# Kernel optimization log

Measured on AMD Instinct MI355X. Metric: run time of the kernel, lower is better.

Reference implementation:

```python
import jax, jax.numpy as jnp
import numpy as np

B, T, E = 2, 2048, 1024
H = 16
D = E // H  # head_dim = 64


def setup_inputs() -> dict:
    key = jax.random.key(0)
    k1, k2, k3 = jax.random.split(key, 3)
    x = jax.random.normal(k1, (B, T, E), dtype=jnp.float32)
    w_qkv = jax.random.normal(k2, (3 * E, E), dtype=jnp.float32) * 0.02
    w_proj = jax.random.normal(k3, (E, E), dtype=jnp.float32) * 0.02
    return {"x": x, "w_qkv": w_qkv, "w_proj": w_proj}


def reference(x, w_qkv, w_proj):
    b, t, c = x.shape
    # qkv projection (torch Linear: x @ W^T), split into q,k,v
    qkv = jnp.einsum('btc,fc->btf', x, w_qkv)  # [B,T,3E]
    q, k, v = jnp.split(qkv, 3, axis=-1)
    # [B,T,E] -> [B,H,T,D]
    q = q.reshape(b, t, H, D).transpose(0, 2, 1, 3)
    k = k.reshape(b, t, H, D).transpose(0, 2, 1, 3)
    v = v.reshape(b, t, H, D).transpose(0, 2, 1, 3)
    scale = 1.0 / jnp.sqrt(jnp.float32(D))
    att = jnp.einsum('bhqd,bhkd->bhqk', q, k) * scale  # [B,H,T,T]
    causal = jnp.tril(jnp.ones((t, t), dtype=bool))
    att = jnp.where(causal[None, None], att, -jnp.inf)
    att = jax.nn.softmax(att, axis=-1)
    out = jnp.einsum('bhqk,bhkd->bhqd', att, v)  # [B,H,T,D]
    out = out.transpose(0, 2, 1, 3).reshape(b, t, c)  # [B,T,E]
    out = jnp.einsum('btc,oc->bto', out, w_proj)
    return out
```

## Files before the change

kernel.cpp:

```cpp
#include <hip/hip_runtime.h>
#include <stdint.h>
#include <stddef.h>

typedef __attribute__((ext_vector_type(8))) short s16x8;
typedef __attribute__((ext_vector_type(4))) short s16x4;
typedef __attribute__((ext_vector_type(4))) float f32x4;

#define B_  2
#define T_  2048
#define E_  1024
#define H_  16
#define E3_ 3072

__device__ __forceinline__ short f2bf(float f) {
  union { float f; uint32_t u; } v; v.f = f;
  uint32_t u = v.u;
  return (short)((u + 0x7FFFu + ((u >> 16) & 1u)) >> 16);
}

__device__ __forceinline__ void gload_lds16(const short* g, short* l) {
  __builtin_amdgcn_global_load_lds(
      (__attribute__((address_space(1))) void*)(const_cast<short*>(g)),
      (__attribute__((address_space(3))) void*)(l), 16, 0, 0);
}

__global__ void castk(const float* __restrict__ in, short* __restrict__ out, int n4) {
  const int i = blockIdx.x * 256 + threadIdx.x;
  if (i >= n4) return;
  const float4 v = ((const float4*)in)[i];
  s16x4 o;
  o[0] = f2bf(v.x); o[1] = f2bf(v.y); o[2] = f2bf(v.z); o[3] = f2bf(v.w);
  ((s16x4*)out)[i] = o;
}

template <int OUT_BF16>
__global__ void gemm_nt_128(const short* __restrict__ A, const short* __restrict__ B,
                            void* __restrict__ Cv, int M, int N, int K) {
  __shared__ short As[128 * 32];
  __shared__ short Bs[128 * 32];
  const int tid  = threadIdx.x;
  const int lane = tid & 63;
  const int w    = tid >> 6;
  const int quad = lane >> 4;
  const int l16  = lane & 15;
  const int wm   = (w >> 1) * 64;
  const int wn   = (w & 1) * 64;
  const int bm   = blockIdx.y * 128;
  const int bn   = blockIdx.x * 128;

  f32x4 acc[4][4];
#pragma unroll
  for (int i = 0; i < 4; i++)
#pragma unroll
    for (int j = 0; j < 4; j++) acc[i][j] = (f32x4){0.f, 0.f, 0.f, 0.f};

  const int srow = w * 32 + (lane >> 2);
  const int scol = (lane & 3) * 8;
  const short* gA = A + (size_t)(bm + srow) * K + scol;
  const short* gB = B + (size_t)(bn + srow) * K + scol;
  short* lA = As + (w * 32) * 32;
  short* lB = Bs + (w * 32) * 32;

  for (int k0 = 0; k0 < K; k0 += 32) {
    __syncthreads();
    gload_lds16(gA + k0,          lA);
    gload_lds16(gA + 16 * K + k0, lA + 16 * 32);
    gload_lds16(gB + k0,          lB);
    gload_lds16(gB + 16 * K + k0, lB + 16 * 32);
    __syncthreads();

    s16x8 a[4], b[4];
#pragma unroll
    for (int i = 0; i < 4; i++)
      a[i] = *(const s16x8*)&As[(wm + i * 16 + l16) * 32 + quad * 8];
#pragma unroll
    for (int j = 0; j < 4; j++)
      b[j] = *(const s16x8*)&Bs[(wn + j * 16 + l16) * 32 + quad * 8];
#pragma unroll
    for (int i = 0; i < 4; i++)
#pragma unroll
      for (int j = 0; j < 4; j++)
        acc[i][j] = __builtin_amdgcn_mfma_f32_16x16x32_bf16(a[i], b[j], acc[i][j], 0, 0, 0);
  }

#pragma unroll
  for (int i = 0; i < 4; i++) {
    const int row0 = bm + wm + i * 16 + quad * 4;
#pragma unroll
    for (int j = 0; j < 4; j++) {
      const int col = bn + wn + j * 16 + l16;
#pragma unroll
      for (int r = 0; r < 4; r++) {
        const size_t idx = (size_t)(row0 + r) * N + col;
        if (OUT_BF16) ((short*)Cv)[idx] = f2bf(acc[i][j][r]);
        else          ((float*)Cv)[idx] = acc[i][j][r];
      }
    }
  }
}

__global__ void vtrans(const short* __restrict__ qkv, short* __restrict__ vt) {
  __shared__ __align__(16) short tile[64 * 68];
  const int tt = blockIdx.x;
  const int bh = blockIdx.y;
  const int b = bh >> 4, h = bh & 15;
  const int tid = threadIdx.x;
#pragma unroll
  for (int k = 0; k < 4; k++) {
    const int c = tid + k * 256;
    const int r = c >> 4;
    const int c4 = (c & 15) * 4;
    s16x4 v = *(const s16x4*)(qkv + (size_t)(b * T_ + tt * 64 + r) * E3_ + 2 * E_ + h * 64 + c4);
    *(s16x4*)&tile[r * 68 + c4] = v;
  }
  __syncthreads();
#pragma unroll
  for (int k = 0; k < 4; k++) {
    const int c = tid + k * 256;
    const int d = c >> 4;
    const int t4 = (c & 15) * 4;
    s16x4 v;
    v[0] = tile[(t4 + 0) * 68 + d];
    v[1] = tile[(t4 + 1) * 68 + d];
    v[2] = tile[(t4 + 2) * 68 + d];
    v[3] = tile[(t4 + 3) * 68 + d];
    *(s16x4*)(vt + (size_t)(bh * 64 + d) * T_ + tt * 64 + t4) = v;
  }
}

__global__ void __launch_bounds__(256, 4)
attn_kernel(const short* __restrict__ qkv, const short* __restrict__ vt,
            short* __restrict__ attout) {
  __shared__ short Ks[2][64 * 64];
  __shared__ short Vs[2][64 * 64];
  __shared__ short Ps[4][16 * 64];
  const int tid  = threadIdx.x;
  const int lane = tid & 63;
  const int w    = tid >> 6;
  const int quad = lane >> 4;
  const int l16  = lane & 15;
  const int bh = blockIdx.x;
  const int b = bh >> 4, h = bh & 15;
  const int qt  = (int)(gridDim.y - 1) - (int)blockIdx.y;
  const int q0b = qt * 64;
  const int q0w = q0b + w * 16;
  const float C1 = 0.18033688011112042f;
  const float NEG_INF = -__builtin_inff();

  const short* qbase = qkv + (size_t)(b * T_ + q0w + l16) * E3_ + h * 64 + quad * 8;
  const s16x8 qf0 = *(const s16x8*)(qbase);
  const s16x8 qf1 = *(const s16x8*)(qbase + 32);

  const int srl = lane >> 3;
  const int sgc = ((lane & 7) ^ srl) * 8;
  const short* gK = qkv + (size_t)(b * T_) * E3_ + E_ + h * 64 + sgc;
  const short* gV = vt + (size_t)(bh * 64) * T_ + sgc;

  f32x4 o[4]; f32x4 s[4];
#pragma unroll
  for (int j = 0; j < 4; j++) o[j] = (f32x4){0.f, 0.f, 0.f, 0.f};
  float l_i[4] = {0.f, 0.f, 0.f, 0.f};
  const int swz = (l16 & 7);

#pragma unroll
  for (int i = 0; i < 2; i++) {
    const int row = w * 16 + i * 8 + srl;
    gload_lds16(gK + (size_t)row * E3_, &Ks[0][(w * 16 + i * 8) * 64]);
    gload_lds16(gV + (size_t)row * T_,  &Vs[0][(w * 16 + i * 8) * 64]);
  }
  __syncthreads();

  for (int kv0 = 0; kv0 <= q0b; kv0 += 64) {
    const int cur = (kv0 >> 6) & 1;

    s16x8 kf[2][4];
#pragma unroll
    for (int c = 0; c < 2; c++)
#pragma unroll
      for (int j = 0; j < 4; j++)
        kf[c][j] = *(const s16x8*)&Ks[cur][(j * 16 + l16) * 64 + (((c * 4 + quad) ^ swz) * 8)];

    if (kv0 + 64 <= q0b) {
#pragma unroll
      for (int i = 0; i < 2; i++) {
        const int row = w * 16 + i * 8 + srl;
        gload_lds16(gK + (size_t)(kv0 + 64 + row) * E3_, &Ks[cur ^ 1][(w * 16 + i * 8) * 64]);
        gload_lds16(gV + (size_t)row * T_ + kv0 + 64,    &Vs[cur ^ 1][(w * 16 + i * 8) * 64]);
      }
    }

#pragma unroll
    for (int j = 0; j < 4; j++) s[j] = (f32x4){0.f, 0.f, 0.f, 0.f};
#pragma unroll
    for (int c = 0; c < 2; c++)
#pragma unroll
      for (int j = 0; j < 4; j++)
        s[j] = __builtin_amdgcn_mfma_f32_16x16x32_bf16(c == 0 ? qf0 : qf1, kf[c][j], s[j], 0, 0, 0);

#pragma unroll
    for (int r = 0; r < 4; r++) {
      const int qa = q0w + quad * 4 + r;
      float v0 = s[0][r], v1 = s[1][r], v2 = s[2][r], v3 = s[3][r];
      if (kv0 + l16 > qa)      v0 = NEG_INF;
      if (kv0 + 16 + l16 > qa) v1 = NEG_INF;
      if (kv0 + 32 + l16 > qa) v2 = NEG_INF;
      if (kv0 + 48 + l16 > qa) v3 = NEG_INF;
      const float p0 = exp2f(v0 * C1);
      const float p1 = exp2f(v1 * C1);
      const float p2 = exp2f(v2 * C1);
      const float p3 = exp2f(v3 * C1);
      l_i[r] += (p0 + p1) + (p2 + p3);
      const int prow = quad * 4 + r;
      const int key  = prow & 7;
      const int lo   = l16 & 7;
      const int hi   = l16 >> 3;
      short* pw = &Ps[w][prow * 64];
      pw[((hi + 0) ^ key) * 8 + lo] = f2bf(p0);
      pw[((hi + 2) ^ key) * 8 + lo] = f2bf(p1);
      pw[((hi + 4) ^ key) * 8 + lo] = f2bf(p2);
      pw[((hi + 6) ^ key) * 8 + lo] = f2bf(p3);
    }
    __asm volatile("s_waitcnt lgkmcnt(0)" ::: "memory");

#pragma unroll
    for (int c = 0; c < 2; c++) {
      const s16x8 pf = *(const s16x8*)&Ps[w][l16 * 64 + (((c * 4 + quad) ^ swz) * 8)];
#pragma unroll
      for (int j = 0; j < 4; j++) {
        const s16x8 vf = *(const s16x8*)&Vs[cur][(j * 16 + l16) * 64 + (((c * 4 + quad) ^ swz) * 8)];
        o[j] = __builtin_amdgcn_mfma_f32_16x16x32_bf16(pf, vf, o[j], 0, 0, 0);
      }
    }

    __syncthreads();
  }

#pragma unroll
  for (int r = 0; r < 4; r++) {
    float rs = l_i[r];
    rs += __shfl_xor(rs, 1);
    rs += __shfl_xor(rs, 2);
    rs += __shfl_xor(rs, 4);
    rs += __shfl_xor(rs, 8);
    const float inv = 1.0f / rs;
    const int q = q0w + quad * 4 + r;
    short* ob = attout + ((size_t)(b * T_ + q) * H_ + h) * 64 + l16;
    ob[0]  = f2bf(o[0][r] * inv);
    ob[16] = f2bf(o[1][r] * inv);
    ob[32] = f2bf(o[2][r] * inv);
    ob[48] = f2bf(o[3][r] * inv);
  }
}

extern "C" void kernel_launch(void* const* d_in, const int* in_sizes, int n_in,
                              void* d_out, int out_size, void* d_ws, size_t ws_size,
                              hipStream_t stream) {
  const float* x     = (const float*)d_in[0];
  const float* wqkv  = (const float*)d_in[1];
  const float* wproj = (const float*)d_in[2];

  if (ws_size < 58720256u) return;
  short* ws     = (short*)d_ws;
  short* xb     = ws;
  short* wqkvb  = xb + 4194304;
  short* wprojb = wqkvb + 3145728;
  short* qkv    = wprojb + 1048576;
  short* vt     = qkv + 12582912;
  short* attb   = vt + 4194304;

  castk<<<4096, 256, 0, stream>>>(x, xb, 1048576);
  castk<<<3072, 256, 0, stream>>>(wqkv, wqkvb, 786432);
  castk<<<1024, 256, 0, stream>>>(wproj, wprojb, 262144);

  gemm_nt_128<1><<<dim3(24, 32), 256, 0, stream>>>(xb, wqkvb, qkv, 4096, 3072, 1024);
  vtrans<<<dim3(32, 32), 256, 0, stream>>>(qkv, vt);
  attn_kernel<<<dim3(32, 32), 256, 0, stream>>>(qkv, vt, attb);
  gemm_nt_128<0><<<dim3(8, 32), 256, 0, stream>>>(attb, wprojb, d_out, 4096, 1024, 1024);
}
```

Baseline: 190.9 us.

## Fold softmax scale into Wq, transpose score MFMA, mask only diagonal, fuse casts

Folds the softmax scale (1/sqrt(D)·log2e) into the Q rows of the QKV weight during the bf16 cast, which removes a multiply per score. The QK^T MFMA is computed transposed so each lane holds contiguous keys for one query. P can then be packed with truncation and written as 64-bit LDS stores, and the row sums reduce with two shuffles plus a small LDS exchange. The causal mask is applied only on the diagonal tile, and the three cast launches are merged into one. P now uses truncation instead of round-to-nearest when converting to bf16, and Q is rounded after scaling, both of which change numerics slightly.

```diff
diff --git a/kernel.cpp b/kernel.cpp
--- a/kernel.cpp
+++ b/kernel.cpp
@@ -18,18 +18,29 @@
   return (short)((u + 0x7FFFu + ((u >> 16) & 1u)) >> 16);
 }
 
+__device__ __forceinline__ uint32_t fbits(float f) {
+  union { float f; uint32_t u; } v; v.f = f; return v.u;
+}
+
 __device__ __forceinline__ void gload_lds16(const short* g, short* l) {
   __builtin_amdgcn_global_load_lds(
       (__attribute__((address_space(1))) void*)(const_cast<short*>(g)),
       (__attribute__((address_space(3))) void*)(l), 16, 0, 0);
 }
 
-__global__ void castk(const float* __restrict__ in, short* __restrict__ out, int n4) {
-  const int i = blockIdx.x * 256 + threadIdx.x;
-  if (i >= n4) return;
+__global__ void castk_all(const float* __restrict__ x, const float* __restrict__ wqkv,
+                          const float* __restrict__ wproj, short* __restrict__ xb,
+                          short* __restrict__ wqkvb, short* __restrict__ wprojb) {
+  const int bid = blockIdx.x;
+  const float* in; short* out; int i; float sc = 1.0f;
+  if (bid < 4096)      { in = x;     out = xb;     i = bid * 256 + threadIdx.x; }
+  else if (bid < 7168) { in = wqkv;  out = wqkvb;  i = (bid - 4096) * 256 + threadIdx.x;
+                         if (i < 262144) sc = 0.18033688011112042f; }
+  else                 { in = wproj; out = wprojb; i = (bid - 7168) * 256 + threadIdx.x; }
   const float4 v = ((const float4*)in)[i];
   s16x4 o;
-  o[0] = f2bf(v.x); o[1] = f2bf(v.y); o[2] = f2bf(v.z); o[3] = f2bf(v.w);
+  o[0] = f2bf(v.x * sc); o[1] = f2bf(v.y * sc);
+  o[2] = f2bf(v.z * sc); o[3] = f2bf(v.w * sc);
   ((s16x4*)out)[i] = o;
 }
 
@@ -134,6 +145,7 @@
   __shared__ short Ks[2][64 * 64];
   __shared__ short Vs[2][64 * 64];
   __shared__ short Ps[4][16 * 64];
+  __shared__ float Ls[4][16];
   const int tid  = threadIdx.x;
   const int lane = tid & 63;
   const int w    = tid >> 6;
@@ -144,7 +156,6 @@
   const int qt  = (int)(gridDim.y - 1) - (int)blockIdx.y;
   const int q0b = qt * 64;
   const int q0w = q0b + w * 16;
-  const float C1 = 0.18033688011112042f;
   const float NEG_INF = -__builtin_inff();
 
   const short* qbase = qkv + (size_t)(b * T_ + q0w + l16) * E3_ + h * 64 + quad * 8;
@@ -156,10 +167,10 @@
   const short* gK = qkv + (size_t)(b * T_) * E3_ + E_ + h * 64 + sgc;
   const short* gV = vt + (size_t)(bh * 64) * T_ + sgc;
 
-  f32x4 o[4]; f32x4 s[4];
+  f32x4 o[4];
 #pragma unroll
   for (int j = 0; j < 4; j++) o[j] = (f32x4){0.f, 0.f, 0.f, 0.f};
-  float l_i[4] = {0.f, 0.f, 0.f, 0.f};
+  float lsum = 0.f;
   const int swz = (l16 & 7);
 
 #pragma unroll
@@ -189,42 +200,41 @@
       }
     }
 
+    f32x4 s[4];
 #pragma unroll
     for (int j = 0; j < 4; j++) s[j] = (f32x4){0.f, 0.f, 0.f, 0.f};
 #pragma unroll
     for (int c = 0; c < 2; c++)
 #pragma unroll
       for (int j = 0; j < 4; j++)
-        s[j] = __builtin_amdgcn_mfma_f32_16x16x32_bf16(c == 0 ? qf0 : qf1, kf[c][j], s[j], 0, 0, 0);
-
-#pragma unroll
-    for (int r = 0; r < 4; r++) {
-      const int qa = q0w + quad * 4 + r;
-      float v0 = s[0][r], v1 = s[1][r], v2 = s[2][r], v3 = s[3][r];
-      if (kv0 + l16 > qa)      v0 = NEG_INF;
-      if (kv0 + 16 + l16 > qa) v1 = NEG_INF;
-      if (kv0 + 32 + l16 > qa) v2 = NEG_INF;
-      if (kv0 + 48 + l16 > qa) v3 = NEG_INF;
-      const float p0 = exp2f(v0 * C1);
-      const float p1 = exp2f(v1 * C1);
-      const float p2 = exp2f(v2 * C1);
-      const float p3 = exp2f(v3 * C1);
-      l_i[r] += (p0 + p1) + (p2 + p3);
-      const int prow = quad * 4 + r;
-      const int key  = prow & 7;
-      const int lo   = l16 & 7;
-      const int hi   = l16 >> 3;
-      short* pw = &Ps[w][prow * 64];
-      pw[((hi + 0) ^ key) * 8 + lo] = f2bf(p0);
-      pw[((hi + 2) ^ key) * 8 + lo] = f2bf(p1);
-      pw[((hi + 4) ^ key) * 8 + lo] = f2bf(p2);
-      pw[((hi + 6) ^ key) * 8 + lo] = f2bf(p3);
+        s[j] = __builtin_amdgcn_mfma_f32_16x16x32_bf16(kf[c][j], c == 0 ? qf0 : qf1, s[j], 0, 0, 0);
+
+    if (kv0 == q0b) {
+#pragma unroll
+      for (int j = 0; j < 4; j++)
+#pragma unroll
+        for (int r = 0; r < 4; r++)
+          if (j * 16 + quad * 4 + r > w * 16 + l16) s[j][r] = NEG_INF;
+    }
+
+#pragma unroll
+    for (int j = 0; j < 4; j++) {
+      const float p0 = exp2f(s[j][0]);
+      const float p1 = exp2f(s[j][1]);
+      const float p2 = exp2f(s[j][2]);
+      const float p3 = exp2f(s[j][3]);
+      lsum += (p0 + p1) + (p2 + p3);
+      int2 pk;
+      pk.x = (int)((fbits(p0) >> 16) | (fbits(p1) & 0xFFFF0000u));
+      pk.y = (int)((fbits(p2) >> 16) | (fbits(p3) & 0xFFFF0000u));
+      short* pw = &Ps[w][l16 * 64 + (((2 * j + (quad >> 1)) ^ swz) * 8) + (quad & 1) * 4];
+      *(int2*)pw = pk;
     }
     __asm volatile("s_waitcnt lgkmcnt(0)" ::: "memory");
 
 #pragma unroll
     for (int c = 0; c < 2; c++) {
-      const s16x8 pf = *(const s16x8*)&Ps[w][l16 * 64 + (((c * 4 + quad) ^ swz) * 8)];
+      const s16x8 pf = *(const s16x8*)&Ps[w][l16 * 64 + (((4 * c + quad) ^ swz) * 8)];
 #pragma unroll
       for (int j = 0; j < 4; j++) {
         const s16x8 vf = *(const s16x8*)&Vs[cur][(j * 16 + l16) * 64 + (((c * 4 + quad) ^ swz) * 8)];
@@ -235,14 +245,14 @@
     __syncthreads();
   }
 
+  lsum += __shfl_xor(lsum, 16);
+  lsum += __shfl_xor(lsum, 32);
+  Ls[w][l16] = lsum;
+  __asm volatile("s_waitcnt lgkmcnt(0)" ::: "memory");
+
 #pragma unroll
   for (int r = 0; r < 4; r++) {
-    float rs = l_i[r];
-    rs += __shfl_xor(rs, 1);
-    rs += __shfl_xor(rs, 2);
-    rs += __shfl_xor(rs, 4);
-    rs += __shfl_xor(rs, 8);
-    const float inv = 1.0f / rs;
+    const float inv = 1.0f / Ls[w][quad * 4 + r];
     const int q = q0w + quad * 4 + r;
     short* ob = attout + ((size_t)(b * T_ + q) * H_ + h) * 64 + l16;
     ob[0]  = f2bf(o[0][r] * inv);
@@ -268,10 +278,7 @@
   short* vt     = qkv + 12582912;
   short* attb   = vt + 4194304;
 
-  castk<<<4096, 256, 0, stream>>>(x, xb, 1048576);
-  castk<<<3072, 256, 0, stream>>>(wqkv, wqkvb, 786432);
-  castk<<<1024, 256, 0, stream>>>(wproj, wprojb, 262144);
-
+  castk_all<<<8192, 256, 0, stream>>>(x, wqkv, wproj, xb, wqkvb, wprojb);
   gemm_nt_128<1><<<dim3(24, 32), 256, 0, stream>>>(xb, wqkvb, qkv, 4096, 3072, 1024);
   vtrans<<<dim3(32, 32), 256, 0, stream>>>(qkv, vt);
   attn_kernel<<<dim3(32, 32), 256, 0, stream>>>(qkv, vt, attb);
```

New measurement: 183.1 us. -4.1%, faster.
